# Kernel optimization log

Measured on AMD Instinct MI355X. Metric: run time of the kernel, lower is better.

The kernel has to match this reference:

```python
import jax, jax.numpy as jnp
import numpy as np

H, W = 512, 512
G = 8192
ALPHA_THRESH = 1.0 / 255.0        # meta_f32[0]
TRANS_THRESH = 1.0e-4             # meta_f32[1]
ALPHA_CAP = 0.99                  # meta_f32[6]
BG = jnp.zeros((3,), dtype=jnp.float32)  # config.background


def setup_inputs() -> dict:
    key = jax.random.key(0)
    ks = jax.random.split(key, 7)
    mx = jax.random.uniform(ks[0], (G,), minval=0.0, maxval=float(W))
    my = jax.random.uniform(ks[1], (G,), minval=0.0, maxval=float(H))
    means2d = jnp.stack([mx, my], axis=-1)
    # Build valid conics (inverse 2x2 covariances) from random rotation + scales
    theta = jax.random.uniform(ks[2], (G,), minval=0.0, maxval=2.0 * np.pi)
    s = jax.random.uniform(ks[3], (G, 2), minval=2.0, maxval=12.0)  # px stddevs
    ct, st = jnp.cos(theta), jnp.sin(theta)
    v1, v2 = s[:, 0] ** 2, s[:, 1] ** 2
    ca = ct * ct * v1 + st * st * v2
    cb = ct * st * (v1 - v2)
    cc = st * st * v1 + ct * ct * v2
    det = ca * cc - cb * cb
    conics = jnp.stack([cc / det, -cb / det, ca / det], axis=-1)  # [G,3] = (a,b,c)
    colors = jax.random.uniform(ks[4], (G, 3))
    opacities = jax.random.uniform(ks[5], (G,))
    depths = jax.random.uniform(ks[6], (G,), minval=0.1, maxval=100.0)
    return {"means2d": means2d, "conics": conics, "colors": colors,
            "opacities": opacities, "depths": depths}


def reference(means2d, conics, colors, opacities, depths):
    # Stable front-to-back depth sort (mirrors perm = argsort(depths, stable))
    perm = jnp.argsort(depths, stable=True)
    m = means2d[perm]
    cn = conics[perm]
    col = colors[perm]
    op = opacities[perm]
    a, b, c = cn[:, 0], cn[:, 1], cn[:, 2]
    px = jnp.arange(W, dtype=means2d.dtype) + 0.5  # pixel centers

    def row(y):
        py = y.astype(means2d.dtype) + 0.5
        dx = px[:, None] - m[None, :, 0]          # [W,G]
        dy = py - m[:, 1]                          # [G]
        sigma = 0.5 * (a * dx * dx + c * dy * dy) + b * dx * dy  # [W,G]
        alpha = jnp.minimum(ALPHA_CAP, op * jnp.exp(-sigma))
        alpha = jnp.where((sigma < 0) | (alpha < ALPHA_THRESH), 0.0, alpha)
        # exclusive cumulative transmittance along depth order
        Tprev = jnp.cumprod(1.0 - alpha, axis=-1)
        Tprev = jnp.concatenate([jnp.ones((W, 1), alpha.dtype), Tprev[:, :-1]], axis=-1)
        # early-termination: splats seen after T drops below threshold contribute 0
        wgt = alpha * Tprev * (Tprev >= TRANS_THRESH)  # [W,G]
        rgb = wgt @ col                                 # [W,3]
        t_rem = 1.0 - wgt.sum(axis=-1)                  # remaining transmittance
        return rgb + t_rem[:, None] * BG

    return jax.lax.map(row, jnp.arange(H))  # [H,W,3]
```

## Files before the change

### kernel.cpp

```cpp
#include <hip/hip_runtime.h>

#define G 8192
#define IMG_W 512
#define IMG_H 512
#define TILE 16
#define NTX (IMG_W / TILE)
#define NTY (IMG_H / TILE)
#define NTILES (NTX * NTY)
#define BLK 256
#define BLKB 64
#define NCHUNK 4
#define CAP 1024
#define ALPHA_THRESH (1.0f/255.0f)
#define ALPHA_CAP 0.99f
#define TRANS_THRESH 1e-4f

#define OFF_TBL   32768
#define OFF_LIST  (OFF_TBL + G*64)
#define OFF_N     (OFF_LIST + NTILES*CAP*2)
#define OFF_PART  (OFF_N + NTILES*4)

__global__ __launch_bounds__(BLK)
void range_kernel(const float* __restrict__ means2d,
                  const float* __restrict__ conics,
                  const float* __restrict__ colors,
                  const float* __restrict__ opac,
                  unsigned int* __restrict__ ranges,
                  float* __restrict__ tbl)
{
    int g = blockIdx.x * BLK + threadIdx.x;
    if (g >= G) return;
    float op = opac[g];
    float a  = conics[3*g], b = conics[3*g+1], c = conics[3*g+2];
    float mx = means2d[2*g], my = means2d[2*g+1];
    float cr = colors[3*g], cg = colors[3*g+1], cb = colors[3*g+2];

    float4* t4 = (float4*)(tbl + (g << 4));
    t4[0] = make_float4(mx, my, 0.5f * a, b);
    t4[1] = make_float4(0.5f * c, op, cr, cg);
    t4[2] = make_float4(cb, 0.0f, 0.0f, 0.0f);

    unsigned int packed = 0xFFu;
    if (op * 255.0f >= 1.0f) {
        float smax = __logf(op * 255.0f);
        float det = fmaxf(a * c - b * b, 1e-12f);
        float rx = sqrtf(fmaxf(2.0f * smax * c / det, 0.0f)) * 1.0001f + 0.01f;
        float ry = sqrtf(fmaxf(2.0f * smax * a / det, 0.0f)) * 1.0001f + 0.01f;
        int txmin = (int)ceilf ((mx - rx - 15.5f) * 0.0625f);
        int txmax = (int)floorf((mx + rx -  0.5f) * 0.0625f);
        int tymin = (int)ceilf ((my - ry - 15.5f) * 0.0625f);
        int tymax = (int)floorf((my + ry -  0.5f) * 0.0625f);
        if (!(txmax < 0 || txmin > NTX-1 || tymax < 0 || tymin > NTY-1 ||
              txmin > txmax || tymin > tymax)) {
            txmin = max(txmin, 0); txmax = min(txmax, NTX-1);
            tymin = max(tymin, 0); tymax = min(tymax, NTY-1);
            packed = (unsigned)txmin | ((unsigned)txmax << 8)
                   | ((unsigned)tymin << 16) | ((unsigned)tymax << 24);
        }
    }
    ranges[g] = packed;
}

__device__ __forceinline__ int hitp(unsigned p, unsigned btx, unsigned bty)
{
    return (btx >= (p & 0xffu)) & (btx <= ((p >> 8) & 0xffu)) &
           (bty >= ((p >> 16) & 0xffu)) & (bty <= (p >> 24));
}

__global__ __launch_bounds__(BLK)
void sort_kernel(const unsigned int* __restrict__ ranges,
                 const float* __restrict__ depths,
                 unsigned short* __restrict__ lists,
                 int* __restrict__ tile_n)
{
    __shared__ __align__(16) unsigned short slist[CAP];
    __shared__ __align__(16) unsigned int fkeys[CAP + 8];
    __shared__ int woff[4];

    const int t = threadIdx.x;
    const int lane = t & 63, w = t >> 6;
    const unsigned btx = blockIdx.x, bty = blockIdx.y;
    const int tile = (int)bty * NTX + (int)btx;

    const uint4* r4 = (const uint4*)ranges;
    const int wbase = w * (G / 4);
    uint4 rv[8];
    #pragma unroll
    for (int i = 0; i < 8; ++i)
        rv[i] = r4[(wbase >> 2) + i * 64 + lane];

    int cnt = 0;
    #pragma unroll
    for (int i = 0; i < 8; ++i)
        cnt += hitp(rv[i].x, btx, bty) + hitp(rv[i].y, btx, bty)
             + hitp(rv[i].z, btx, bty) + hitp(rv[i].w, btx, bty);
    #pragma unroll
    for (int d = 1; d < 64; d <<= 1) cnt += __shfl_xor(cnt, d);
    if (lane == 0) woff[w] = cnt;
    __syncthreads();

    int offs = 0;
    for (int ww = 0; ww < w; ++ww) offs += woff[ww];
    const int N = min(woff[0] + woff[1] + woff[2] + woff[3], CAP);

    const unsigned long long lt = (1ull << lane) - 1ull;
    #pragma unroll
    for (int i = 0; i < 8; ++i) {
        int gbase = wbase + i * 256 + lane * 4;
        int h0 = hitp(rv[i].x, btx, bty), h1 = hitp(rv[i].y, btx, bty);
        int h2 = hitp(rv[i].z, btx, bty), h3 = hitp(rv[i].w, btx, bty);
        unsigned long long m0 = __ballot(h0), m1 = __ballot(h1);
        unsigned long long m2 = __ballot(h2), m3 = __ballot(h3);
        int pos = offs + __popcll(m0 & lt) + __popcll(m1 & lt)
                       + __popcll(m2 & lt) + __popcll(m3 & lt);
        if (h0) { if (pos < CAP) slist[pos] = (unsigned short)(gbase    ); pos++; }
        if (h1) { if (pos < CAP) slist[pos] = (unsigned short)(gbase + 1); pos++; }
        if (h2) { if (pos < CAP) slist[pos] = (unsigned short)(gbase + 2); pos++; }
        if (h3) { if (pos < CAP) slist[pos] = (unsigned short)(gbase + 3); pos++; }
        offs += __popcll(m0) + __popcll(m1) + __popcll(m2) + __popcll(m3);
    }
    __syncthreads();

    unsigned short myidx[4]; unsigned int mykey[4]; int myr[4];
    #pragma unroll
    for (int m = 0; m < 4; ++m) {
        int i = t + m * BLK;
        if (i < N) {
            unsigned idx = slist[i];
            unsigned k = __float_as_uint(depths[idx]);
            myidx[m] = (unsigned short)idx; mykey[m] = k; fkeys[i] = k;
        }
    }
    if (t < 8) fkeys[N + t] = 0xFFFFFFFFu;
    __syncthreads();

    const uint4* fk4 = (const uint4*)fkeys;
    const int nj4 = (N + 3) >> 2;
    #pragma unroll
    for (int m = 0; m < 4; ++m) {
        int i = t + m * BLK;
        if (i < N) {
            unsigned ke = mykey[m]; int r = 0;
            for (int j4 = 0; j4 < nj4; ++j4) {
                uint4 kv = fk4[j4]; int j = j4 << 2;
                r += (int)((kv.x < ke) | ((kv.x == ke) & (j     < i)));
                r += (int)((kv.y < ke) | ((kv.y == ke) & (j + 1 < i)));
                r += (int)((kv.z < ke) | ((kv.z == ke) & (j + 2 < i)));
                r += (int)((kv.w < ke) | ((kv.w == ke) & (j + 3 < i)));
            }
            myr[m] = r;
        }
    }
    __syncthreads();
    #pragma unroll
    for (int m = 0; m < 4; ++m) {
        int i = t + m * BLK;
        if (i < N) slist[myr[m]] = myidx[m];
    }
    __syncthreads();

    for (int i = t; i < N; i += BLK) lists[tile * CAP + i] = slist[i];
    if (t == 0) tile_n[tile] = N;
}

__global__ __launch_bounds__(BLKB)
void chunk_kernel(const unsigned short* __restrict__ lists,
                  const int* __restrict__ tile_n,
                  const float* __restrict__ tbl,
                  float4* __restrict__ partials)
{
    __shared__ float4 sq0[BLKB];
    __shared__ float4 sq1[BLKB];
    __shared__ float  sq2[BLKB];

    const int bx = blockIdx.x;
    const int tile = bx >> 2, chunk = bx & 3;
    const int l = threadIdx.x;
    const int n = tile_n[tile];
    const int csz = (n + NCHUNK - 1) >> 2;
    const int cs = chunk * csz;
    const int ce = min(n, cs + csz);

    const int tx = tile & (NTX - 1), ty = tile >> 5;
    const float px  = (float)(tx * TILE + (l & 15)) + 0.5f;
    const int   y0  = (l >> 4) << 2;
    const float py0 = (float)(ty * TILE + y0) + 0.5f;
    const float py1 = py0 + 1.0f, py2 = py0 + 2.0f, py3 = py0 + 3.0f;

    float T0=1.f,T1=1.f,T2=1.f,T3=1.f;
    float ar0=0.f,ag0=0.f,ab0=0.f, ar1=0.f,ag1=0.f,ab1=0.f;
    float ar2=0.f,ag2=0.f,ab2=0.f, ar3=0.f,ag3=0.f,ab3=0.f;

    for (int base = cs; base < ce; base += BLKB) {
        int k = min(BLKB, ce - base);
        float4 v0 = make_float4(0.f,0.f,0.f,0.f);
        float4 v1 = make_float4(0.f,0.f,0.f,0.f);
        float  v2 = 0.f;
        if (l < k) {
            int idx = lists[tile * CAP + base + l];
            const float4* b = (const float4*)(tbl + (idx << 4));
            v0 = b[0]; v1 = b[1]; v2 = ((const float*)b)[8];
        }
        __syncthreads();
        sq0[l] = v0; sq1[l] = v1; sq2[l] = v2;
        __syncthreads();

        int k4 = (k + 3) & ~3;
        bool fin = false;
        for (int i = 0; i < k4; i += 4) {
            #pragma unroll
            for (int u = 0; u < 4; ++u) {
                float4 q0 = sq0[i + u];
                float4 q1 = sq1[i + u];
                float  bl = sq2[i + u];
                float dx = px - q0.x;
                float dxdx = dx * dx;
                float dy0 = py0 - q0.y, dy1 = py1 - q0.y;
                float dy2 = py2 - q0.y, dy3 = py3 - q0.y;
                float sg0 = fmaf(q0.z, dxdx, fmaf(q1.x, dy0*dy0, q0.w*(dx*dy0)));
                float sg1 = fmaf(q0.z, dxdx, fmaf(q1.x, dy1*dy1, q0.w*(dx*dy1)));
                float sg2 = fmaf(q0.z, dxdx, fmaf(q1.x, dy2*dy2, q0.w*(dx*dy2)));
                float sg3 = fmaf(q0.z, dxdx, fmaf(q1.x, dy3*dy3, q0.w*(dx*dy3)));
                float al0 = q1.y * __expf(-sg0);
                float al1 = q1.y * __expf(-sg1);
                float al2 = q1.y * __expf(-sg2);
                float al3 = q1.y * __expf(-sg3);
                al0 = ((sg0 >= 0.f) && (al0 >= ALPHA_THRESH)) ? fminf(al0, ALPHA_CAP) : 0.f;
                al1 = ((sg1 >= 0.f) && (al1 >= ALPHA_THRESH)) ? fminf(al1, ALPHA_CAP) : 0.f;
                al2 = ((sg2 >= 0.f) && (al2 >= ALPHA_THRESH)) ? fminf(al2, ALPHA_CAP) : 0.f;
                al3 = ((sg3 >= 0.f) && (al3 >= ALPHA_THRESH)) ? fminf(al3, ALPHA_CAP) : 0.f;
                float w0 = al0*T0, w1 = al1*T1, w2 = al2*T2, w3 = al3*T3;
                ar0 = fmaf(w0, q1.z, ar0);  ar1 = fmaf(w1, q1.z, ar1);
                ar2 = fmaf(w2, q1.z, ar2);  ar3 = fmaf(w3, q1.z, ar3);
                ag0 = fmaf(w0, q1.w, ag0);  ag1 = fmaf(w1, q1.w, ag1);
                ag2 = fmaf(w2, q1.w, ag2);  ag3 = fmaf(w3, q1.w, ag3);
                ab0 = fmaf(w0, bl,   ab0);  ab1 = fmaf(w1, bl,   ab1);
                ab2 = fmaf(w2, bl,   ab2);  ab3 = fmaf(w3, bl,   ab3);
                T0 *= (1.f - al0);
                T1 *= (1.f - al1);
                T2 *= (1.f - al2);
                T3 *= (1.f - al3);
            }
            if (__all((T0 < TRANS_THRESH) & (T1 < TRANS_THRESH) &
                      (T2 < TRANS_THRESH) & (T3 < TRANS_THRESH))) {
                fin = true; break;
            }
        }
        if (fin) break;
    }

    float4* p = partials + ((long)bx << 8);
    const int xl = l & 15;
    p[(y0    ) * 16 + xl] = make_float4(ar0, ag0, ab0, T0);
    p[(y0 + 1) * 16 + xl] = make_float4(ar1, ag1, ab1, T1);
    p[(y0 + 2) * 16 + xl] = make_float4(ar2, ag2, ab2, T2);
    p[(y0 + 3) * 16 + xl] = make_float4(ar3, ag3, ab3, T3);
}

__global__ __launch_bounds__(BLK)
void merge_kernel(const float4* __restrict__ partials,
                  float* __restrict__ out)
{
    int px = blockIdx.x * BLK + threadIdx.x;
    int X = px & (IMG_W - 1), Y = px >> 9;
    int tile = (Y >> 4) * NTX + (X >> 4);
    int widx = (Y & 15) * 16 + (X & 15);
    const float4* base = partials + ((long)tile << 10);
    float4 p0 = base[widx];
    float4 p1 = base[256 + widx];
    float4 p2 = base[512 + widx];
    float4 p3 = base[768 + widx];
    float r = p3.x, g = p3.y, b = p3.z;
    r = fmaf(p2.w, r, p2.x); g = fmaf(p2.w, g, p2.y); b = fmaf(p2.w, b, p2.z);
    r = fmaf(p1.w, r, p1.x); g = fmaf(p1.w, g, p1.y); b = fmaf(p1.w, b, p1.z);
    r = fmaf(p0.w, r, p0.x); g = fmaf(p0.w, g, p0.y); b = fmaf(p0.w, b, p0.z);
    out[px*3]     = r;
    out[px*3 + 1] = g;
    out[px*3 + 2] = b;
}

extern "C" void kernel_launch(void* const* d_in, const int* in_sizes, int n_in,
                              void* d_out, int out_size, void* d_ws, size_t ws_size,
                              hipStream_t stream)
{
    const float* means2d = (const float*)d_in[0];
    const float* conics  = (const float*)d_in[1];
    const float* colors  = (const float*)d_in[2];
    const float* opac    = (const float*)d_in[3];
    const float* depths  = (const float*)d_in[4];
    float* out = (float*)d_out;

    unsigned int*   ranges   = (unsigned int*)d_ws;
    float*          tbl      = (float*)((char*)d_ws + OFF_TBL);
    unsigned short* lists    = (unsigned short*)((char*)d_ws + OFF_LIST);
    int*            tile_n   = (int*)((char*)d_ws + OFF_N);
    float4*         partials = (float4*)((char*)d_ws + OFF_PART);

    range_kernel<<<G / BLK, BLK, 0, stream>>>(means2d, conics, colors, opac,
                                              ranges, tbl);
    sort_kernel<<<dim3(NTX, NTY), BLK, 0, stream>>>(ranges, depths,
                                                    lists, tile_n);
    chunk_kernel<<<NTILES * NCHUNK, BLKB, 0, stream>>>(lists, tile_n,
                                                       tbl, partials);
    merge_kernel<<<(IMG_W * IMG_H) / BLK, BLK, 0, stream>>>(partials, out);
}
```

Measured before the change: 102.0 us.

## Fuse sort, chunk render and merge into a single per-tile kernel

Merges the sort, chunk and merge kernels into one per-tile kernel. Each of the four wavefronts renders one depth chunk of the tile's sorted list straight from shared memory, and the partial results are composited in shared memory. This removes two kernel launches and the global round-trips for the per-tile lists and partials. In exchange, parallelism drops from 4096 small blocks to 1024 blocks of 256 threads, shared memory per block grows, and the waves within a block can be imbalanced.

After: 87.08 us. -14.6%, faster.

```diff
diff --git a/kernel.cpp b/kernel.cpp
--- a/kernel.cpp
+++ b/kernel.cpp
@@ -6,19 +6,12 @@
 #define TILE 16
 #define NTX (IMG_W / TILE)
 #define NTY (IMG_H / TILE)
-#define NTILES (NTX * NTY)
 #define BLK 256
 #define BLKB 64
-#define NCHUNK 4
 #define CAP 1024
 #define ALPHA_THRESH (1.0f/255.0f)
 #define ALPHA_CAP 0.99f
 #define TRANS_THRESH 1e-4f
-
-#define OFF_TBL   32768
-#define OFF_LIST  (OFF_TBL + G*64)
-#define OFF_N     (OFF_LIST + NTILES*CAP*2)
-#define OFF_PART  (OFF_N + NTILES*4)
 
 __global__ __launch_bounds__(BLK)
 void range_kernel(const float* __restrict__ means2d,
@@ -68,19 +61,22 @@
 }
 
 __global__ __launch_bounds__(BLK)
-void sort_kernel(const unsigned int* __restrict__ ranges,
+void tile_kernel(const unsigned int* __restrict__ ranges,
                  const float* __restrict__ depths,
-                 unsigned short* __restrict__ lists,
-                 int* __restrict__ tile_n)
+                 const float* __restrict__ tbl,
+                 float*       __restrict__ out)
 {
     __shared__ __align__(16) unsigned short slist[CAP];
     __shared__ __align__(16) unsigned int fkeys[CAP + 8];
     __shared__ int woff[4];
+    __shared__ float4 sq0[4][BLKB];
+    __shared__ float4 sq1[4][BLKB];
+    __shared__ float  sq2[4][BLKB];
+    __shared__ float4 part[4][BLK];
 
     const int t = threadIdx.x;
     const int lane = t & 63, w = t >> 6;
     const unsigned btx = blockIdx.x, bty = blockIdx.y;
-    const int tile = (int)bty * NTX + (int)btx;
 
     const uint4* r4 = (const uint4*)ranges;
     const int wbase = w * (G / 4);
@@ -159,32 +155,13 @@
     }
     __syncthreads();
 
-    for (int i = t; i < N; i += BLK) lists[tile * CAP + i] = slist[i];
-    if (t == 0) tile_n[tile] = N;
-}
-
-__global__ __launch_bounds__(BLKB)
-void chunk_kernel(const unsigned short* __restrict__ lists,
-                  const int* __restrict__ tile_n,
-                  const float* __restrict__ tbl,
-                  float4* __restrict__ partials)
-{
-    __shared__ float4 sq0[BLKB];
-    __shared__ float4 sq1[BLKB];
-    __shared__ float  sq2[BLKB];
-
-    const int bx = blockIdx.x;
-    const int tile = bx >> 2, chunk = bx & 3;
-    const int l = threadIdx.x;
-    const int n = tile_n[tile];
-    const int csz = (n + NCHUNK - 1) >> 2;
-    const int cs = chunk * csz;
-    const int ce = min(n, cs + csz);
-
-    const int tx = tile & (NTX - 1), ty = tile >> 5;
-    const float px  = (float)(tx * TILE + (l & 15)) + 0.5f;
-    const int   y0  = (l >> 4) << 2;
-    const float py0 = (float)(ty * TILE + y0) + 0.5f;
+    const int csz = (N + 3) >> 2;
+    const int cs = w * csz;
+    const int ce = min(N, cs + csz);
+
+    const float px  = (float)(btx * TILE + (lane & 15)) + 0.5f;
+    const int   y0  = (lane >> 4) << 2;
+    const float py0 = (float)(bty * TILE + y0) + 0.5f;
     const float py1 = py0 + 1.0f, py2 = py0 + 2.0f, py3 = py0 + 3.0f;
 
     float T0=1.f,T1=1.f,T2=1.f,T3=1.f;
@@ -196,23 +173,22 @@
         float4 v0 = make_float4(0.f,0.f,0.f,0.f);
         float4 v1 = make_float4(0.f,0.f,0.f,0.f);
         float  v2 = 0.f;
-        if (l < k) {
-            int idx = lists[tile * CAP + base + l];
+        if (lane < k) {
+            int idx = slist[base + lane];
             const float4* b = (const float4*)(tbl + (idx << 4));
             v0 = b[0]; v1 = b[1]; v2 = ((const float*)b)[8];
         }
-        __syncthreads();
-        sq0[l] = v0; sq1[l] = v1; sq2[l] = v2;
-        __syncthreads();
+        sq0[w][lane] = v0; sq1[w][lane] = v1; sq2[w][lane] = v2;
+        __threadfence_block();
 
         int k4 = (k + 3) & ~3;
         bool fin = false;
         for (int i = 0; i < k4; i += 4) {
             #pragma unroll
             for (int u = 0; u < 4; ++u) {
-                float4 q0 = sq0[i + u];
-                float4 q1 = sq1[i + u];
-                float  bl = sq2[i + u];
+                float4 q0 = sq0[w][i + u];
+                float4 q1 = sq1[w][i + u];
+                float  bl = sq2[w][i + u];
                 float dx = px - q0.x;
                 float dxdx = dx * dx;
                 float dy0 = py0 - q0.y, dy1 = py1 - q0.y;
@@ -249,34 +225,27 @@
         if (fin) break;
     }
 
-    float4* p = partials + ((long)bx << 8);
-    const int xl = l & 15;
-    p[(y0    ) * 16 + xl] = make_float4(ar0, ag0, ab0, T0);
-    p[(y0 + 1) * 16 + xl] = make_float4(ar1, ag1, ab1, T1);
-    p[(y0 + 2) * 16 + xl] = make_float4(ar2, ag2, ab2, T2);
-    p[(y0 + 3) * 16 + xl] = make_float4(ar3, ag3, ab3, T3);
-}
-
-__global__ __launch_bounds__(BLK)
-void merge_kernel(const float4* __restrict__ partials,
-                  float* __restrict__ out)
-{
-    int px = blockIdx.x * BLK + threadIdx.x;
-    int X = px & (IMG_W - 1), Y = px >> 9;
-    int tile = (Y >> 4) * NTX + (X >> 4);
-    int widx = (Y & 15) * 16 + (X & 15);
-    const float4* base = partials + ((long)tile << 10);
-    float4 p0 = base[widx];
-    float4 p1 = base[256 + widx];
-    float4 p2 = base[512 + widx];
-    float4 p3 = base[768 + widx];
+    {
+        const int xl = lane & 15;
+        part[w][(y0    ) * 16 + xl] = make_float4(ar0, ag0, ab0, T0);
+        part[w][(y0 + 1) * 16 + xl] = make_float4(ar1, ag1, ab1, T1);
+        part[w][(y0 + 2) * 16 + xl] = make_float4(ar2, ag2, ab2, T2);
+        part[w][(y0 + 3) * 16 + xl] = make_float4(ar3, ag3, ab3, T3);
+    }
+    __syncthreads();
+
+    float4 p0 = part[0][t], p1 = part[1][t], p2 = part[2][t], p3 = part[3][t];
     float r = p3.x, g = p3.y, b = p3.z;
     r = fmaf(p2.w, r, p2.x); g = fmaf(p2.w, g, p2.y); b = fmaf(p2.w, b, p2.z);
     r = fmaf(p1.w, r, p1.x); g = fmaf(p1.w, g, p1.y); b = fmaf(p1.w, b, p1.z);
     r = fmaf(p0.w, r, p0.x); g = fmaf(p0.w, g, p0.y); b = fmaf(p0.w, b, p0.z);
-    out[px*3]     = r;
-    out[px*3 + 1] = g;
-    out[px*3 + 2] = b;
+
+    const int X = (int)btx * TILE + (t & 15);
+    const int Y = (int)bty * TILE + (t >> 4);
+    const int o = (Y * IMG_W + X) * 3;
+    out[o]     = r;
+    out[o + 1] = g;
+    out[o + 2] = b;
 }
 
 extern "C" void kernel_launch(void* const* d_in, const int* in_sizes, int n_in,
@@ -289,18 +258,11 @@
     const float* opac    = (const float*)d_in[3];
     const float* depths  = (const float*)d_in[4];
     float* out = (float*)d_out;
-
-    unsigned int*   ranges   = (unsigned int*)d_ws;
-    float*          tbl      = (float*)((char*)d_ws + OFF_TBL);
-    unsigned short* lists    = (unsigned short*)((char*)d_ws + OFF_LIST);
-    int*            tile_n   = (int*)((char*)d_ws + OFF_N);
-    float4*         partials = (float4*)((char*)d_ws + OFF_PART);
+    unsigned int* ranges = (unsigned int*)d_ws;
+    float* tbl = (float*)((char*)d_ws + 32 * 1024);
 
     range_kernel<<<G / BLK, BLK, 0, stream>>>(means2d, conics, colors, opac,
                                               ranges, tbl);
-    sort_kernel<<<dim3(NTX, NTY), BLK, 0, stream>>>(ranges, depths,
-                                                    lists, tile_n);
-    chunk_kernel<<<NTILES * NCHUNK, BLKB, 0, stream>>>(lists, tile_n,
-                                                       tbl, partials);
-    merge_kernel<<<(IMG_W * IMG_H) / BLK, BLK, 0, stream>>>(partials, out);
-}
+    tile_kernel<<<dim3(NTX, NTY), dim3(BLK), 0, stream>>>(
+        ranges, depths, tbl, out);
+}
```
